# Performance work log

Measured on AMD Instinct MI355X. Metric: run time of the kernel, lower is better.

Reference implementation:

```python
import jax, jax.numpy as jnp
import numpy as np

Q_OFFSET = 128  # stored quants are in [0,255); subtract to get signed int8 range


def setup_inputs() -> dict:
    key = jax.random.key(0)
    k1, k2, k3, k4 = jax.random.split(key, 4)
    O, NB, BS = 4096, 128, 32  # out_features, num_blocks, block_size (Q8_0)
    x = jax.random.normal(k1, (4, 1024, NB * BS), dtype=jnp.float16)
    q_weight = jax.random.randint(k2, (O, NB, BS), 0, 255, dtype=jnp.int32)
    scales = jax.random.uniform(k3, (O, NB), dtype=jnp.float16) * jnp.float16(0.05)
    bias = jax.random.normal(k4, (O,), dtype=jnp.float16)
    return {"x": x, "q_weight": q_weight, "scales": scales, "bias": bias}


def reference(x, q_weight, scales, bias):
    # GGUF Q8_0-style on-the-fly dequant: w[o, b*32+j] = (q[o,b,j]-128) * scale[o,b]
    q = q_weight.astype(jnp.float16) - jnp.float16(Q_OFFSET)  # [O, NB, BS]
    w = (q * scales[:, :, None]).reshape(scales.shape[0], -1)  # [O, I]
    # linear: y = x @ w^T + bias
    return jnp.einsum('bsi,oi->bso', x, w) + bias
```

## Files before the change

kernel.cpp:

```cpp
#include <hip/hip_runtime.h>
#include <stdint.h>


#define QOFF 128

typedef __bf16 bf16_t;
typedef __bf16 bf16x8 __attribute__((ext_vector_type(8)));
typedef float f32x4 __attribute__((ext_vector_type(4)));

#define W_VM4 0x0F74
#define W_VM0 0x0F70

__global__ __launch_bounds__(256) void prep_kernel(
    const int* __restrict__ q, const float* __restrict__ scales,
    const float* __restrict__ X, bf16_t* __restrict__ W,
    bf16_t* __restrict__ Xb, int K, int NB, int nDeq) {
  const int b = blockIdx.x;
  if (b < nDeq) {
    const size_t e = ((size_t)b * 256 + threadIdx.x) * 8;
    const int o = (int)(e / (size_t)K);
    const int i = (int)(e % (size_t)K);
    const float s = scales[o * NB + (i >> 5)];
    int4 a = *(const int4*)(q + e);
    int4 c = *(const int4*)(q + e + 4);
    const int* av = (const int*)&a;
    const int* cv = (const int*)&c;
    bf16x8 t;
#pragma unroll
    for (int j = 0; j < 4; ++j) t[j] = (bf16_t)((float)(av[j] - QOFF) * s);
#pragma unroll
    for (int j = 0; j < 4; ++j) t[4 + j] = (bf16_t)((float)(cv[j] - QOFF) * s);
    *(bf16x8*)(W + e) = t;
  } else {
    const size_t e = ((size_t)(b - nDeq) * 256 + threadIdx.x) * 8;
    float4 a = *(const float4*)(X + e);
    float4 c = *(const float4*)(X + e + 4);
    bf16x8 t;
    t[0] = (bf16_t)a.x; t[1] = (bf16_t)a.y; t[2] = (bf16_t)a.z; t[3] = (bf16_t)a.w;
    t[4] = (bf16_t)c.x; t[5] = (bf16_t)c.y; t[6] = (bf16_t)c.z; t[7] = (bf16_t)c.w;
    *(bf16x8*)(Xb + e) = t;
  }
}

__device__ __forceinline__ void async16(bf16_t* lds, const bf16_t* g) {
  __builtin_amdgcn_global_load_lds(
      (const __attribute__((address_space(1))) unsigned int*)(const void*)g,
      (__attribute__((address_space(3))) unsigned int*)(void*)lds, 16, 0, 0);
}

template <int QM, int QN>
__device__ __forceinline__ void mm_block(f32x4 (&acc)[8][4],
                                         const bf16x8 (&af)[4][2],
                                         const bf16x8 (&bv)[2][2]) {
  __builtin_amdgcn_s_setprio(1);
#pragma unroll
  for (int ks = 0; ks < 2; ++ks)
#pragma unroll
    for (int fi = 0; fi < 4; ++fi)
#pragma unroll
      for (int fj = 0; fj < 2; ++fj)
        acc[QM * 4 + fi][QN * 2 + fj] = __builtin_amdgcn_mfma_f32_16x16x32_bf16(
            af[fi][ks], bv[fj][ks], acc[QM * 4 + fi][QN * 2 + fj], 0, 0, 0);
  __builtin_amdgcn_s_setprio(0);
}

__device__ __forceinline__ void rd_a(const bf16_t* base, const int* swz,
                                     bf16x8 (&af)[4][2]) {
#pragma unroll
  for (int ks = 0; ks < 2; ++ks)
#pragma unroll
    for (int fi = 0; fi < 4; ++fi)
      af[fi][ks] = *(const bf16x8*)(base + fi * 1024 + swz[ks]);
}

__device__ __forceinline__ void rd_b(const bf16_t* base, const int* swz,
                                     bf16x8 (&bv)[2][2]) {
#pragma unroll
  for (int ks = 0; ks < 2; ++ks)
#pragma unroll
    for (int fj = 0; fj < 2; ++fj)
      bv[fj][ks] = *(const bf16x8*)(base + fj * 1024 + swz[ks]);
}

__device__ __forceinline__ void rd12(const bf16_t* abase, const bf16_t* bbase,
                                     const int* swz, bf16x8 (&af)[4][2],
                                     bf16x8 (&bv)[2][2]) {
#pragma unroll
  for (int ks = 0; ks < 2; ++ks) {
    af[0][ks] = *(const bf16x8*)(abase + swz[ks]);
    bv[0][ks] = *(const bf16x8*)(bbase + swz[ks]);
    af[1][ks] = *(const bf16x8*)(abase + 1024 + swz[ks]);
    bv[1][ks] = *(const bf16x8*)(bbase + 1024 + swz[ks]);
    af[2][ks] = *(const bf16x8*)(abase + 2048 + swz[ks]);
    af[3][ks] = *(const bf16x8*)(abase + 3072 + swz[ks]);
  }
}

__global__ __launch_bounds__(512, 2) void gemm_8ph(
    const bf16_t* __restrict__ A,
    const bf16_t* __restrict__ B,
    const float* __restrict__ bias,
    float* __restrict__ C,
    int M, int N, int K) {
  __shared__ bf16_t lsA[2][256 * 64];
  __shared__ bf16_t lsB[2][256 * 64];

  const int tid = threadIdx.x;
  const int lane = tid & 63;
  const int wave = tid >> 6;
  const int r = lane & 15;
  const int qd = lane >> 4;
  const int wm = (wave >> 2) * 128;
  const int wn = (wave & 3) * 64;

  const int nbx = N >> 8;
  const int nwg = gridDim.x;
  int wg = blockIdx.x;
  if ((nwg & 7) == 0) wg = (wg & 7) * (nwg >> 3) + (wg >> 3);
  const int m0 = (wg / nbx) * 256;
  const int n0 = (wg % nbx) * 256;

  f32x4 acc[8][4] = {};

  const int srow = tid >> 3;
  const int sslot = (tid & 7) ^ (srow & 7);
  const bf16_t* gA0 = A + (size_t)(m0 + srow) * K + sslot * 8;
  const bf16_t* gB0 = B + (size_t)(n0 + srow) * K + sslot * 8;

  auto stgA = [&](bf16_t* dstTile, int half, int koff) {
    bf16_t* d = dstTile + half * 8192 + tid * 8;
    const bf16_t* g = gA0 + (size_t)(half * 128) * K + koff;
    async16(d, g);
    async16(d + 4096, g + 64 * (size_t)K);
  };
  auto stgB = [&](bf16_t* dstTile, int half, int koff) {
    bf16_t* d = dstTile + half * 8192 + tid * 8;
    const bf16_t* g = gB0 + (size_t)(half * 128) * K + koff;
    async16(d, g);
    async16(d + 4096, g + 64 * (size_t)K);
  };

  const int swz[2] = {(qd ^ (r & 7)) * 8, ((4 + qd) ^ (r & 7)) * 8};
  const bf16_t* a0base = &lsA[0][(wm + r) * 64];
  const bf16_t* a1base = &lsA[1][(wm + r) * 64];
  const bf16_t* b0base = &lsB[0][(wn + r) * 64];
  const bf16_t* b1base = &lsB[1][(wn + r) * 64];

  const int NT = K >> 6;

  bf16x8 af_lo[4][2], af_hi[4][2], bv0[2][2], bv1[2][2];

  stgA(lsA[0], 0, 0);
  stgA(lsA[0], 1, 0);
  stgB(lsB[0], 0, 0);
  stgB(lsB[0], 1, 0);
  stgA(lsA[1], 0, 64);
  stgA(lsA[1], 1, 64);
  __builtin_amdgcn_s_waitcnt(W_VM4);
  __builtin_amdgcn_s_barrier();
  rd12(a0base, b0base, swz, af_lo, bv0);
  stgB(lsB[1], 0, 64);
  stgB(lsB[1], 1, 64);

#define TILE_STEP(CUR, NXT, K2)                                       \
             \
  rd_a(a##CUR##base + 4096, swz, af_hi);                              \
  rd_b(b##CUR##base + 2048, swz, bv1);                                \
  mm_block<0, 0>(acc, af_lo, bv0);                                    \
  mm_block<1, 0>(acc, af_hi, bv0);                                    \
  __builtin_amdgcn_s_barrier();                               \
                                                              \
  stgA(lsA[CUR], 0, K2);                                              \
  stgA(lsA[CUR], 1, K2);                                              \
  mm_block<0, 1>(acc, af_lo, bv1);                                    \
  __builtin_amdgcn_s_waitcnt(W_VM4);                                  \
  __builtin_amdgcn_s_barrier();                               \
                                                              \
  rd12(a##NXT##base, b##NXT##base, swz, af_lo, bv0);                  \
  stgB(lsB[CUR], 0, K2);                                              \
  stgB(lsB[CUR], 1, K2);                                              \
  mm_block<1, 1>(acc, af_hi, bv1);

#pragma unroll 1
  for (int j = 0; j < NT / 2; ++j) {
    int t2 = 2 * j + 2; if (t2 >= NT) t2 -= NT;
    int t3 = 2 * j + 3; if (t3 >= NT) t3 -= NT;
    const int k2 = t2 * 64;
    const int k3 = t3 * 64;
    TILE_STEP(0, 1, k2)
    TILE_STEP(1, 0, k3)
  }
#undef TILE_STEP

  __builtin_amdgcn_s_waitcnt(W_VM0);

#pragma unroll
  for (int ni = 0; ni < 4; ++ni) {
    const int n = n0 + wn + ni * 16 + r;
    const float bv = bias[n];
#pragma unroll
    for (int mi = 0; mi < 8; ++mi) {
      const int mbase = m0 + wm + mi * 16 + qd * 4;
#pragma unroll
      for (int reg = 0; reg < 4; ++reg) {
        C[(size_t)(mbase + reg) * N + n] = acc[mi][ni][reg] + bv;
      }
    }
  }
}

__global__ __launch_bounds__(256) void gemm_db(
    const bf16_t* __restrict__ A, const bf16_t* __restrict__ B,
    const float* __restrict__ bias, float* __restrict__ C, int M, int N,
    int K) {
  __shared__ bf16_t lsA[2][128 * 32];
  __shared__ bf16_t lsB[2][128 * 32];

  const int tid = threadIdx.x;
  const int lane = tid & 63;
  const int wave = tid >> 6;
  const int m0 = blockIdx.y * 128;
  const int n0 = blockIdx.x * 128;
  const int wm = (wave >> 1) * 64;
  const int wn = (wave & 1) * 64;
  const int r = lane & 15;
  const int qd = lane >> 4;

  f32x4 acc[4][4] = {};

  const int e0 = tid * 8;
  const int e1 = 2048 + tid * 8;
  const bf16_t* gA0 = A + (size_t)(m0 + (e0 >> 5)) * K + (e0 & 31);
  const bf16_t* gA1 = A + (size_t)(m0 + (e1 >> 5)) * K + (e1 & 31);
  const bf16_t* gB0 = B + (size_t)(n0 + (e0 >> 5)) * K + (e0 & 31);
  const bf16_t* gB1 = B + (size_t)(n0 + (e1 >> 5)) * K + (e1 & 31);

  async16(&lsA[0][e0], gA0);
  async16(&lsA[0][e1], gA1);
  async16(&lsB[0][e0], gB0);
  async16(&lsB[0][e1], gB1);

  int buf = 0;
  for (int k0 = 0; k0 < K; k0 += 32, buf ^= 1) {
    __syncthreads();
    if (k0 + 32 < K) {
      const int nk = k0 + 32;
      async16(&lsA[buf ^ 1][e0], gA0 + nk);
      async16(&lsA[buf ^ 1][e1], gA1 + nk);
      async16(&lsB[buf ^ 1][e0], gB0 + nk);
      async16(&lsB[buf ^ 1][e1], gB1 + nk);
    }
    bf16x8 af[4], bfv[4];
#pragma unroll
    for (int i = 0; i < 4; ++i) {
      af[i] = *(const bf16x8*)&lsA[buf][(wm + i * 16 + r) * 32 + qd * 8];
      bfv[i] = *(const bf16x8*)&lsB[buf][(wn + i * 16 + r) * 32 + qd * 8];
    }
#pragma unroll
    for (int mi = 0; mi < 4; ++mi)
#pragma unroll
      for (int ni = 0; ni < 4; ++ni)
        acc[mi][ni] = __builtin_amdgcn_mfma_f32_16x16x32_bf16(
            af[mi], bfv[ni], acc[mi][ni], 0, 0, 0);
  }

#pragma unroll
  for (int ni = 0; ni < 4; ++ni) {
    const int n = n0 + wn + ni * 16 + r;
    const float bv = bias[n];
#pragma unroll
    for (int mi = 0; mi < 4; ++mi) {
      const int mbase = m0 + wm + mi * 16 + qd * 4;
#pragma unroll
      for (int reg = 0; reg < 4; ++reg) {
        C[(size_t)(mbase + reg) * N + n] = acc[mi][ni][reg] + bv;
      }
    }
  }
}

__global__ __launch_bounds__(256) void gemm_fused(
    const float* __restrict__ Af, const int* __restrict__ q,
    const float* __restrict__ scales, const float* __restrict__ bias,
    float* __restrict__ C, int M, int N, int K, int NB) {
  __shared__ bf16_t lsA[128 * 32];
  __shared__ bf16_t lsB[128 * 32];

  const int tid = threadIdx.x;
  const int lane = tid & 63;
  const int wave = tid >> 6;
  const int m0 = blockIdx.y * 128;
  const int n0 = blockIdx.x * 128;
  const int wm = (wave >> 1) * 64;
  const int wn = (wave & 1) * 64;
  const int r = lane & 15;
  const int qd = lane >> 4;

  const int e = tid * 16;
  const int row = e >> 5;
  const int col = e & 31;

  const float* gAf = Af + (size_t)(m0 + row) * K + col;
  const int* gQ = q + (size_t)(n0 + row) * K + col;
  const float* gS = scales + (size_t)(n0 + row) * NB;

  f32x4 acc[4][4] = {};

  for (int k0 = 0; k0 < K; k0 += 32) {
    bf16x8 a0, a1, b0, b1;
    {
      float4 f0 = *(const float4*)(gAf + k0);
      float4 f1 = *(const float4*)(gAf + k0 + 4);
      float4 f2 = *(const float4*)(gAf + k0 + 8);
      float4 f3 = *(const float4*)(gAf + k0 + 12);
      a0[0] = (bf16_t)f0.x; a0[1] = (bf16_t)f0.y; a0[2] = (bf16_t)f0.z; a0[3] = (bf16_t)f0.w;
      a0[4] = (bf16_t)f1.x; a0[5] = (bf16_t)f1.y; a0[6] = (bf16_t)f1.z; a0[7] = (bf16_t)f1.w;
      a1[0] = (bf16_t)f2.x; a1[1] = (bf16_t)f2.y; a1[2] = (bf16_t)f2.z; a1[3] = (bf16_t)f2.w;
      a1[4] = (bf16_t)f3.x; a1[5] = (bf16_t)f3.y; a1[6] = (bf16_t)f3.z; a1[7] = (bf16_t)f3.w;
    }
    {
      const float s = gS[k0 >> 5];
      int qv[16];
      *(int4*)&qv[0] = *(const int4*)(gQ + k0);
      *(int4*)&qv[4] = *(const int4*)(gQ + k0 + 4);
      *(int4*)&qv[8] = *(const int4*)(gQ + k0 + 8);
      *(int4*)&qv[12] = *(const int4*)(gQ + k0 + 12);
#pragma unroll
      for (int j = 0; j < 8; ++j) b0[j] = (bf16_t)((float)(qv[j] - QOFF) * s);
#pragma unroll
      for (int j = 0; j < 8; ++j)
        b1[j] = (bf16_t)((float)(qv[8 + j] - QOFF) * s);
    }

    __syncthreads();
    *(bf16x8*)&lsA[e] = a0;
    *(bf16x8*)&lsA[e + 8] = a1;
    *(bf16x8*)&lsB[e] = b0;
    *(bf16x8*)&lsB[e + 8] = b1;
    __syncthreads();

    bf16x8 af[4], bfv[4];
#pragma unroll
    for (int i = 0; i < 4; ++i) {
      af[i] = *(const bf16x8*)&lsA[(wm + i * 16 + r) * 32 + qd * 8];
      bfv[i] = *(const bf16x8*)&lsB[(wn + i * 16 + r) * 32 + qd * 8];
    }
#pragma unroll
    for (int mi = 0; mi < 4; ++mi)
#pragma unroll
      for (int ni = 0; ni < 4; ++ni)
        acc[mi][ni] = __builtin_amdgcn_mfma_f32_16x16x32_bf16(
            af[mi], bfv[ni], acc[mi][ni], 0, 0, 0);
  }

#pragma unroll
  for (int ni = 0; ni < 4; ++ni) {
    const int n = n0 + wn + ni * 16 + r;
    const float bv = bias[n];
#pragma unroll
    for (int mi = 0; mi < 4; ++mi) {
      const int mbase = m0 + wm + mi * 16 + qd * 4;
#pragma unroll
      for (int reg = 0; reg < 4; ++reg) {
        C[(size_t)(mbase + reg) * N + n] = acc[mi][ni][reg] + bv;
      }
    }
  }
}

extern "C" void kernel_launch(void* const* d_in, const int* in_sizes, int n_in,
                              void* d_out, int out_size, void* d_ws,
                              size_t ws_size, hipStream_t stream) {
  const float* x = (const float*)d_in[0];
  const int* qw = (const int*)d_in[1];
  const float* scales = (const float*)d_in[2];
  const float* bias = (const float*)d_in[3];
  float* out = (float*)d_out;

  const int O = in_sizes[3];
  const int K = in_sizes[1] / O;
  const int NB = in_sizes[2] / O;
  const int M = in_sizes[0] / K;
  (void)n_in; (void)out_size;

  const size_t Wbytes = (size_t)O * K * sizeof(bf16_t);
  const size_t Xbytes = (size_t)M * K * sizeof(bf16_t);

  if (ws_size >= Wbytes + Xbytes) {
    bf16_t* W = (bf16_t*)d_ws;
    bf16_t* Xb = (bf16_t*)((char*)d_ws + Wbytes);
    const int nDeq = (int)((size_t)O * K / 2048);
    const int nCvt = (int)((size_t)M * K / 2048);
    prep_kernel<<<nDeq + nCvt, 256, 0, stream>>>(qw, scales, x, W, Xb, K, NB,
                                                 nDeq);
    if ((M % 256) == 0 && (O % 256) == 0 && (K % 128) == 0) {
      const int nwg = (M / 256) * (O / 256);
      gemm_8ph<<<nwg, 512, 0, stream>>>(Xb, W, bias, out, M, O, K);
    } else {
      dim3 grid(O / 128, M / 128);
      gemm_db<<<grid, 256, 0, stream>>>(Xb, W, bias, out, M, O, K);
    }
  } else {
    dim3 grid(O / 128, M / 128);
    gemm_fused<<<grid, 256, 0, stream>>>(x, qw, scales, bias, out, M, O, K,
                                         NB);
  }
}
```

Before: 289.8 us.

## Switch GEMM inner loop from 16x16x32 to 32x32x16 bf16 MFMA tiles

Reworks the 8-phase GEMM so each wave's 128x64 sub-tile is covered by 32x32x16 MFMA instructions instead of 16x16x32 ones. LDS fragment reads, swizzle offsets, accumulator layout and the epilogue store mapping are rewritten to match the 32x32 output layout. Larger MFMA tiles cut the number of LDS fragment reads per FLOP and the instruction-issue overhead. In exchange, the epilogue store pattern changes and the per-instruction latency is longer, which may alter how well loads interleave with MFMA work.

```diff
diff --git a/kernel.cpp b/kernel.cpp
--- a/kernel.cpp
+++ b/kernel.cpp
@@ -7,6 +7,7 @@
 typedef __bf16 bf16_t;
 typedef __bf16 bf16x8 __attribute__((ext_vector_type(8)));
 typedef float f32x4 __attribute__((ext_vector_type(4)));
+typedef float f32x16 __attribute__((ext_vector_type(16)));
 
 #define W_VM4 0x0F74
 #define W_VM0 0x0F70
@@ -49,50 +50,43 @@
 }
 
 template <int QM, int QN>
-__device__ __forceinline__ void mm_block(f32x4 (&acc)[8][4],
-                                         const bf16x8 (&af)[4][2],
-                                         const bf16x8 (&bv)[2][2]) {
+__device__ __forceinline__ void mm_block(f32x16 (&acc)[4][2],
+                                         const bf16x8 (&af)[2][4],
+                                         const bf16x8 (&bv)[4]) {
   __builtin_amdgcn_s_setprio(1);
 #pragma unroll
-  for (int ks = 0; ks < 2; ++ks)
-#pragma unroll
-    for (int fi = 0; fi < 4; ++fi)
-#pragma unroll
-      for (int fj = 0; fj < 2; ++fj)
-        acc[QM * 4 + fi][QN * 2 + fj] = __builtin_amdgcn_mfma_f32_16x16x32_bf16(
-            af[fi][ks], bv[fj][ks], acc[QM * 4 + fi][QN * 2 + fj], 0, 0, 0);
+  for (int ks = 0; ks < 4; ++ks)
+#pragma unroll
+    for (int mi = 0; mi < 2; ++mi)
+      acc[QM * 2 + mi][QN] = __builtin_amdgcn_mfma_f32_32x32x16_bf16(
+          af[mi][ks], bv[ks], acc[QM * 2 + mi][QN], 0, 0, 0);
   __builtin_amdgcn_s_setprio(0);
 }
 
 __device__ __forceinline__ void rd_a(const bf16_t* base, const int* swz,
-                                     bf16x8 (&af)[4][2]) {
-#pragma unroll
-  for (int ks = 0; ks < 2; ++ks)
-#pragma unroll
-    for (int fi = 0; fi < 4; ++fi)
-      af[fi][ks] = *(const bf16x8*)(base + fi * 1024 + swz[ks]);
+                                     bf16x8 (&af)[2][4]) {
+#pragma unroll
+  for (int ks = 0; ks < 4; ++ks)
+#pragma unroll
+    for (int mi = 0; mi < 2; ++mi)
+      af[mi][ks] = *(const bf16x8*)(base + mi * 2048 + swz[ks]);
 }
 
 __device__ __forceinline__ void rd_b(const bf16_t* base, const int* swz,
-                                     bf16x8 (&bv)[2][2]) {
-#pragma unroll
-  for (int ks = 0; ks < 2; ++ks)
-#pragma unroll
-    for (int fj = 0; fj < 2; ++fj)
-      bv[fj][ks] = *(const bf16x8*)(base + fj * 1024 + swz[ks]);
+                                     bf16x8 (&bv)[4]) {
+#pragma unroll
+  for (int ks = 0; ks < 4; ++ks)
+    bv[ks] = *(const bf16x8*)(base + swz[ks]);
 }
 
 __device__ __forceinline__ void rd12(const bf16_t* abase, const bf16_t* bbase,
-                                     const int* swz, bf16x8 (&af)[4][2],
-                                     bf16x8 (&bv)[2][2]) {
-#pragma unroll
-  for (int ks = 0; ks < 2; ++ks) {
+                                     const int* swz, bf16x8 (&af)[2][4],
+                                     bf16x8 (&bv)[4]) {
+#pragma unroll
+  for (int ks = 0; ks < 4; ++ks) {
     af[0][ks] = *(const bf16x8*)(abase + swz[ks]);
-    bv[0][ks] = *(const bf16x8*)(bbase + swz[ks]);
-    af[1][ks] = *(const bf16x8*)(abase + 1024 + swz[ks]);
-    bv[1][ks] = *(const bf16x8*)(bbase + 1024 + swz[ks]);
-    af[2][ks] = *(const bf16x8*)(abase + 2048 + swz[ks]);
-    af[3][ks] = *(const bf16x8*)(abase + 3072 + swz[ks]);
+    bv[ks] = *(const bf16x8*)(bbase + swz[ks]);
+    af[1][ks] = *(const bf16x8*)(abase + 2048 + swz[ks]);
   }
 }
 
@@ -108,8 +102,8 @@
   const int tid = threadIdx.x;
   const int lane = tid & 63;
   const int wave = tid >> 6;
-  const int r = lane & 15;
-  const int qd = lane >> 4;
+  const int r32 = lane & 31;
+  const int q2 = lane >> 5;
   const int wm = (wave >> 2) * 128;
   const int wn = (wave & 3) * 64;
 
@@ -120,7 +114,7 @@
   const int m0 = (wg / nbx) * 256;
   const int n0 = (wg % nbx) * 256;
 
-  f32x4 acc[8][4] = {};
+  f32x16 acc[4][2] = {};
 
   const int srow = tid >> 3;
   const int sslot = (tid & 7) ^ (srow & 7);
@@ -140,15 +134,18 @@
     async16(d + 4096, g + 64 * (size_t)K);
   };
 
-  const int swz[2] = {(qd ^ (r & 7)) * 8, ((4 + qd) ^ (r & 7)) * 8};
-  const bf16_t* a0base = &lsA[0][(wm + r) * 64];
-  const bf16_t* a1base = &lsA[1][(wm + r) * 64];
-  const bf16_t* b0base = &lsB[0][(wn + r) * 64];
-  const bf16_t* b1base = &lsB[1][(wn + r) * 64];
+  const int swz[4] = {((0 * 2 + q2) ^ (r32 & 7)) * 8,
+                      ((1 * 2 + q2) ^ (r32 & 7)) * 8,
+                      ((2 * 2 + q2) ^ (r32 & 7)) * 8,
+                      ((3 * 2 + q2) ^ (r32 & 7)) * 8};
+  const bf16_t* a0base = &lsA[0][(wm + r32) * 64];
+  const bf16_t* a1base = &lsA[1][(wm + r32) * 64];
+  const bf16_t* b0base = &lsB[0][(wn + r32) * 64];
+  const bf16_t* b1base = &lsB[1][(wn + r32) * 64];
 
   const int NT = K >> 6;
 
-  bf16x8 af_lo[4][2], af_hi[4][2], bv0[2][2], bv1[2][2];
+  bf16x8 af_lo[2][4], af_hi[2][4], bv0[4], bv1[4];
 
   stgA(lsA[0], 0, 0);
   stgA(lsA[0], 1, 0);
@@ -194,16 +191,18 @@
 
   __builtin_amdgcn_s_waitcnt(W_VM0);
 
-#pragma unroll
-  for (int ni = 0; ni < 4; ++ni) {
-    const int n = n0 + wn + ni * 16 + r;
-    const float bv = bias[n];
-#pragma unroll
-    for (int mi = 0; mi < 8; ++mi) {
-      const int mbase = m0 + wm + mi * 16 + qd * 4;
-#pragma unroll
-      for (int reg = 0; reg < 4; ++reg) {
-        C[(size_t)(mbase + reg) * N + n] = acc[mi][ni][reg] + bv;
+  const int hi4 = q2 * 4;
+#pragma unroll
+  for (int nj = 0; nj < 2; ++nj) {
+    const int n = n0 + wn + nj * 32 + r32;
+    const float bvs = bias[n];
+#pragma unroll
+    for (int mi = 0; mi < 4; ++mi) {
+      const int mb = m0 + wm + mi * 32 + hi4;
+#pragma unroll
+      for (int reg = 0; reg < 16; ++reg) {
+        const int m = mb + (reg & 3) + 8 * (reg >> 2);
+        C[(size_t)m * N + n] = acc[mi][nj][reg] + bvs;
       }
     }
   }
```

Result: slower. 307.0 us (+5.9%).
